# Kernel tuning notes

Measured on AMD Instinct MI355X. Metric: run time of the kernel, lower is better.

Reference implementation:

```python
import jax, jax.numpy as jnp
import numpy as np

D_MODEL = 1024
N_HEADS = 16
HEAD_DIM = D_MODEL // N_HEADS
NEG_INF = -1e9


def setup_inputs() -> dict:
    key = jax.random.key(0)
    ks = jax.random.split(key, 6)
    B, T, C = 4, 2048, D_MODEL
    x = jax.random.normal(ks[0], (B, T, C), dtype=jnp.float32)
    # causal mask, broadcastable over batch and heads
    mask = jnp.tril(jnp.ones((T, T), dtype=jnp.int32))[None, None]
    scale = 1.0 / np.sqrt(C)
    W_qkv = jax.random.normal(ks[1], (3 * C, C), dtype=jnp.float32) * scale
    b_qkv = jnp.zeros((3 * C,), dtype=jnp.float32)
    W_out = jax.random.normal(ks[2], (C, C), dtype=jnp.float32) * scale
    b_out = jnp.zeros((C,), dtype=jnp.float32)
    return {"x": x, "mask": mask, "W_qkv": W_qkv, "b_qkv": b_qkv,
            "W_out": W_out, "b_out": b_out}


def reference(x, mask, W_qkv, b_qkv, W_out, b_out):
    B, T, C = x.shape
    H, D = N_HEADS, HEAD_DIM
    qkv = x @ W_qkv.T + b_qkv                      # [B, T, 3C]
    q, k, v = jnp.split(qkv, 3, axis=-1)
    # [B, T, C] -> [B, H, T, D]
    q = q.reshape(B, T, H, D).transpose(0, 2, 1, 3)
    k = k.reshape(B, T, H, D).transpose(0, 2, 1, 3)
    v = v.reshape(B, T, H, D).transpose(0, 2, 1, 3)
    scores = jnp.einsum("bhqd,bhkd->bhqk", q, k) / np.sqrt(D)
    scores = jnp.where(mask == 0, NEG_INF, scores)
    att = jax.nn.softmax(scores, axis=-1)          # dropout p=0 (eval)
    out = jnp.einsum("bhqk,bhkd->bhqd", att, v)    # [B, H, T, D]
    out = out.transpose(0, 2, 1, 3).reshape(B, T, C)
    return out @ W_out.T + b_out
```

## Files before the change

kernel.cpp:

```cpp
#include <hip/hip_runtime.h>
#include <hip/hip_bf16.h>

typedef unsigned short u16;
typedef unsigned int u32;
using short8 = __attribute__((ext_vector_type(8))) short;
using f32x4  = __attribute__((ext_vector_type(4))) float;
using f32x16 = __attribute__((ext_vector_type(16))) float;
using uint2v = __attribute__((ext_vector_type(2))) u32;

#define T_SEQ 2048
#define C_DIM 1024
#define NH 16
#define HD 64

#if __has_builtin(__builtin_amdgcn_exp2f)
#define EXP2(x) __builtin_amdgcn_exp2f(x)
#else
#define EXP2(x) exp2f(x)
#endif

__device__ __forceinline__ u16 f2bf(float f) {
    unsigned int u = __float_as_uint(f);
    unsigned int r = (u + 0x7fffu + ((u >> 16) & 1u)) >> 16;
    return (u16)r;
}
__device__ __forceinline__ u32 cvtpk(float lo, float hi) {
    u32 r;
    asm("v_cvt_pk_bf16_f32 %0, %1, %2" : "=v"(r) : "v"(lo), "v"(hi));
    return r;
}
__device__ __forceinline__ short8 mk8(u32 a, u32 b, u32 c, u32 d) {
    union { u32 u[4]; short8 s; } t;
    t.u[0] = a; t.u[1] = b; t.u[2] = c; t.u[3] = d;
    return t.s;
}
__device__ __forceinline__ void gl_lds16(const u16* g, u16* l) {
    __builtin_amdgcn_global_load_lds(
        (const __attribute__((address_space(1))) unsigned int*)g,
        (__attribute__((address_space(3))) unsigned int*)l, 16, 0, 0);
}
template <int N> __device__ __forceinline__ void s_vmcnt();
template <> __device__ __forceinline__ void s_vmcnt<0>() {
    asm volatile("s_waitcnt vmcnt(0)" ::: "memory");
}
template <> __device__ __forceinline__ void s_vmcnt<4>() {
    asm volatile("s_waitcnt vmcnt(4)" ::: "memory");
}
__device__ __forceinline__ void BAR() {
    asm volatile("" ::: "memory");
    __builtin_amdgcn_s_barrier();
    asm volatile("" ::: "memory");
}

__global__ __launch_bounds__(256) void cvt_f32_bf16(const float* __restrict__ in,
                                                    u16* __restrict__ out, int n8) {
    int i = blockIdx.x * blockDim.x + threadIdx.x;
    if (i >= n8) return;
    const float4* p = (const float4*)in + (size_t)i * 2;
    float4 a = p[0], b = p[1];
    short8 o;
    o[0] = (short)f2bf(a.x); o[1] = (short)f2bf(a.y);
    o[2] = (short)f2bf(a.z); o[3] = (short)f2bf(a.w);
    o[4] = (short)f2bf(b.x); o[5] = (short)f2bf(b.y);
    o[6] = (short)f2bf(b.z); o[7] = (short)f2bf(b.w);
    *(short8*)(out + (size_t)i * 8) = o;
}

__global__ __launch_bounds__(256) void cvt_w2(const float* __restrict__ a,
                                              u16* __restrict__ oa, int na8,
                                              const float* __restrict__ b,
                                              u16* __restrict__ ob, int nb8) {
    int i = blockIdx.x * blockDim.x + threadIdx.x;
    const float* src;
    u16* dst;
    if (i < na8) { src = a; dst = oa; }
    else if (i < na8 + nb8) { src = b; dst = ob; i -= na8; }
    else return;
    const float4* p = (const float4*)src + (size_t)i * 2;
    float4 x = p[0], y = p[1];
    short8 o;
    o[0] = (short)f2bf(x.x); o[1] = (short)f2bf(x.y);
    o[2] = (short)f2bf(x.z); o[3] = (short)f2bf(x.w);
    o[4] = (short)f2bf(y.x); o[5] = (short)f2bf(y.y);
    o[6] = (short)f2bf(y.z); o[7] = (short)f2bf(y.w);
    *(short8*)(dst + (size_t)i * 8) = o;
}

template <int EPI, int NX>
__global__ __launch_bounds__(256) void gemm_bt(const u16* __restrict__ A,
                                               const u16* __restrict__ Bt,
                                               const float* __restrict__ bias,
                                               u16* __restrict__ qb, u16* __restrict__ kb,
                                               u16* __restrict__ vtb, float* __restrict__ Cf,
                                               int M, int N, int K) {
    __shared__ __align__(16) u16 Al[2][128][32];
    __shared__ __align__(16) u16 Bl[2][128][32];
    const int tid = threadIdx.x;
    const int lane = tid & 63, wid = tid >> 6;
    const int li = lane & 15, g = lane >> 4;
    const int wr = (wid >> 1) * 64, wc = (wid & 1) * 64;

    const int bid = blockIdx.x;
    const int xcd = bid & 7;
    const int r_ = bid >> 3;
    const int xq = r_ >> 5;
    const int rem = r_ & 31;
    const int yloc = rem >> 2, xr = rem & 3;
    const size_t m0 = (size_t)(xcd * 8 + yloc) * 128;
    const size_t n0 = (size_t)(xq * 4 + xr) * 128;

    const int srow = lane >> 2;
    const int sch = (lane & 3) ^ ((srow >> 1) & 3);
    const u16* aA = A + (m0 + wid * 32 + srow) * (size_t)K + sch * 8;
    const u16* aB = Bt + (n0 + wid * 32 + srow) * (size_t)K + sch * 8;

    f32x4 acc[4][4] = {};
    const int nt = K / 32;

    auto STAGE = [&](int buf, int k0) {
        gl_lds16(aA + k0, &Al[buf][wid * 32][0]);
        gl_lds16(aA + 16 * (size_t)K + k0, &Al[buf][wid * 32 + 16][0]);
        gl_lds16(aB + k0, &Bl[buf][wid * 32][0]);
        gl_lds16(aB + 16 * (size_t)K + k0, &Bl[buf][wid * 32 + 16][0]);
    };

    STAGE(0, 0);
#pragma unroll 2
    for (int t = 0; t < nt; ++t) {
        if (t + 1 < nt) { STAGE((t + 1) & 1, (t + 1) * 32); s_vmcnt<4>(); }
        else            { s_vmcnt<0>(); }
        BAR();
        short8 af[4], bf[4];
#pragma unroll
        for (int i = 0; i < 4; i++) {
            int row = wr + i * 16 + li;
            af[i] = *(const short8*)&Al[t & 1][row][(g ^ ((row >> 1) & 3)) * 8];
        }
#pragma unroll
        for (int i = 0; i < 4; i++) {
            int row = wc + i * 16 + li;
            bf[i] = *(const short8*)&Bl[t & 1][row][(g ^ ((row >> 1) & 3)) * 8];
        }
        __builtin_amdgcn_s_setprio(1);
#pragma unroll
        for (int mi = 0; mi < 4; mi++)
#pragma unroll
            for (int ni = 0; ni < 4; ni++)
                acc[mi][ni] = __builtin_amdgcn_mfma_f32_16x16x32_bf16(af[mi], bf[ni],
                                                                      acc[mi][ni], 0, 0, 0);
        __builtin_amdgcn_s_setprio(0);
        BAR();
    }

#pragma unroll
    for (int mi = 0; mi < 4; mi++)
#pragma unroll
        for (int ni = 0; ni < 4; ni++) {
            size_t col = n0 + wc + ni * 16 + li;
            size_t row0 = m0 + wr + mi * 16 + g * 4;
            if (EPI == 0) {
                int which = (int)(col >> 10);
                int rem2 = (int)(col & 1023);
                int h = rem2 >> 6, d = rem2 & 63;
                size_t b = row0 >> 11, t0v = row0 & 2047;
                float bv = bias[col];
                if (which == 2) {
                    ushort4 o4;
                    o4.x = f2bf(acc[mi][ni][0] + bv);
                    o4.y = f2bf(acc[mi][ni][1] + bv);
                    o4.z = f2bf(acc[mi][ni][2] + bv);
                    o4.w = f2bf(acc[mi][ni][3] + bv);
                    *(ushort4*)(vtb + (((b * NH) + h) * (size_t)HD + d) * T_SEQ + t0v) = o4;
                } else {
                    u16* dst = (which == 0) ? qb : kb;
                    float sc = (which == 0) ? 0.18033688f : 1.0f;
#pragma unroll
                    for (int r = 0; r < 4; r++)
                        dst[(((b * NH) + h) * T_SEQ + t0v + r) * HD + d] =
                            f2bf((acc[mi][ni][r] + bv) * sc);
                }
            } else {
                float bv = bias[col];
#pragma unroll
                for (int r = 0; r < 4; r++)
                    Cf[(row0 + r) * (size_t)N + col] = acc[mi][ni][r] + bv;
            }
        }
}

__global__ __launch_bounds__(256) void attn_fwd2(const u16* __restrict__ Q,
                                                 const u16* __restrict__ K,
                                                 const u16* __restrict__ Vt,
                                                 u16* __restrict__ O) {
    __shared__ __align__(16) u16 KL[2][64 * 64];
    __shared__ __align__(16) u16 VL[2][64 * 64];
    const int tid = threadIdx.x;
    const int lane = tid & 63, wid = tid >> 6;
    const int l31 = lane & 31, hi = lane >> 5;

    const int wg = blockIdx.x;
    const int j = wg >> 8, c = wg & 255;
    const int xcd = c & 7, m = c >> 3;
    const int bh = (xcd << 3) | (m >> 2);
    const int v = m & 3;
    const int qt = (j == 0) ? (15 - v) : (j == 1) ? v : (j == 2) ? (11 - v) : (v + 4);

    const size_t bhT = (size_t)bh * T_SEQ;
    const int srow8 = lane >> 3, sch = lane & 7;
    const int b = bh >> 4, h = bh & 15;
    const int x7 = l31 & 7;

    const int q0 = qt * 128;
    const int qw0 = q0 + wid * 32;
    const int nkt = 2 * qt + 2;

    short8 qf[4];
    {
        const u16* qp = Q + (bhT + qw0 + l31) * HD + hi * 8;
#pragma unroll
        for (int s = 0; s < 4; s++) qf[s] = *(const short8*)(qp + s * 16);
    }

    f32x16 o0 = {}, o1 = {};
    float l_run = 0.f;

#pragma unroll
    for (int i = 0; i < 2; i++) {
        int row = wid * 16 + i * 8 + srow8;
        int ch = sch ^ (row & 7);
        gl_lds16(K + (bhT + row) * HD + ch * 8, &KL[0][(wid * 16 + i * 8) * 64]);
        gl_lds16(Vt + ((size_t)bh * HD + row) * T_SEQ + ch * 8,
                 &VL[0][(wid * 16 + i * 8) * 64]);
    }

    for (int kt = 0; kt < nkt; kt++) {
        if (kt + 1 < nkt) {
            const int kv0n = (kt + 1) * 64;
            const int nb = (kt + 1) & 1;
#pragma unroll
            for (int i = 0; i < 2; i++) {
                int row = wid * 16 + i * 8 + srow8;
                int ch = sch ^ (row & 7);
                gl_lds16(K + (bhT + kv0n + row) * HD + ch * 8,
                         &KL[nb][(wid * 16 + i * 8) * 64]);
                gl_lds16(Vt + ((size_t)bh * HD + row) * T_SEQ + kv0n + ch * 8,
                         &VL[nb][(wid * 16 + i * 8) * 64]);
            }
            s_vmcnt<4>();
        } else {
            s_vmcnt<0>();
        }
        BAR();

        const int kv0 = kt * 64;
        if (kv0 <= qw0) {
            const u16* KLb = KL[kt & 1];
            const u16* VLb = VL[kt & 1];

            f32x16 s0 = {}, s1 = {};
            __builtin_amdgcn_s_setprio(1);
#pragma unroll
            for (int sl = 0; sl < 4; sl++) {
                int ch = ((sl * 2 + hi) ^ x7) * 8;
                short8 ka = *(const short8*)&KLb[l31 * 64 + ch];
                s0 = __builtin_amdgcn_mfma_f32_32x32x16_bf16(ka, qf[sl], s0, 0, 0, 0);
                short8 kb2 = *(const short8*)&KLb[(32 + l31) * 64 + ch];
                s1 = __builtin_amdgcn_mfma_f32_32x32x16_bf16(kb2, qf[sl], s1, 0, 0, 0);
            }
            __builtin_amdgcn_s_setprio(0);

            const int qg = qw0 + l31;
            if (kv0 + 63 > qw0) {
#pragma unroll
                for (int r = 0; r < 16; r++) {
                    int kvr = kv0 + (r & 3) + 8 * (r >> 2) + 4 * hi;
                    if (kvr > qg) s0[r] = -1e30f;
                    if (kvr + 32 > qg) s1[r] = -1e30f;
                }
            }

            float ls = 0.f;
#pragma unroll
            for (int r = 0; r < 16; r++) {
                float p0 = EXP2(s0[r]);
                float p1 = EXP2(s1[r]);
                s0[r] = p0; s1[r] = p1;
                ls += p0 + p1;
            }
            ls += __shfl_xor(ls, 32);
            l_run += ls;

            {
                u32 c0 = cvtpk(s0[0], s0[1]),   c1 = cvtpk(s0[2], s0[3]),
                    c2 = cvtpk(s0[4], s0[5]),   c3 = cvtpk(s0[6], s0[7]),
                    c4 = cvtpk(s0[8], s0[9]),   c5 = cvtpk(s0[10], s0[11]),
                    c6 = cvtpk(s0[12], s0[13]), c7 = cvtpk(s0[14], s0[15]);
                uint2v wA = __builtin_amdgcn_permlane32_swap(c0, c2, false, false);
                uint2v wB = __builtin_amdgcn_permlane32_swap(c1, c3, false, false);
                uint2v wC = __builtin_amdgcn_permlane32_swap(c4, c6, false, false);
                uint2v wD = __builtin_amdgcn_permlane32_swap(c5, c7, false, false);
                short8 paA = mk8(wA[0], wB[0], wA[1], wB[1]);
                short8 paB = mk8(wC[0], wD[0], wC[1], wD[1]);
                __builtin_amdgcn_s_setprio(1);
#pragma unroll
                for (int sl = 0; sl < 2; sl++) {
                    short8 pa = (sl == 0) ? paA : paB;
                    int ch = ((sl * 2 + hi) ^ x7) * 8;
                    short8 va = *(const short8*)&VLb[l31 * 64 + ch];
                    o0 = __builtin_amdgcn_mfma_f32_32x32x16_bf16(pa, va, o0, 0, 0, 0);
                    short8 vb2 = *(const short8*)&VLb[(32 + l31) * 64 + ch];
                    o1 = __builtin_amdgcn_mfma_f32_32x32x16_bf16(pa, vb2, o1, 0, 0, 0);
                }
                __builtin_amdgcn_s_setprio(0);
            }
            {
                u32 c0 = cvtpk(s1[0], s1[1]),   c1 = cvtpk(s1[2], s1[3]),
                    c2 = cvtpk(s1[4], s1[5]),   c3 = cvtpk(s1[6], s1[7]),
                    c4 = cvtpk(s1[8], s1[9]),   c5 = cvtpk(s1[10], s1[11]),
                    c6 = cvtpk(s1[12], s1[13]), c7 = cvtpk(s1[14], s1[15]);
                uint2v wA = __builtin_amdgcn_permlane32_swap(c0, c2, false, false);
                uint2v wB = __builtin_amdgcn_permlane32_swap(c1, c3, false, false);
                uint2v wC = __builtin_amdgcn_permlane32_swap(c4, c6, false, false);
                uint2v wD = __builtin_amdgcn_permlane32_swap(c5, c7, false, false);
                short8 paC = mk8(wA[0], wB[0], wA[1], wB[1]);
                short8 paD = mk8(wC[0], wD[0], wC[1], wD[1]);
                __builtin_amdgcn_s_setprio(1);
#pragma unroll
                for (int sl = 2; sl < 4; sl++) {
                    short8 pa = (sl == 2) ? paC : paD;
                    int ch = ((sl * 2 + hi) ^ x7) * 8;
                    short8 va = *(const short8*)&VLb[l31 * 64 + ch];
                    o0 = __builtin_amdgcn_mfma_f32_32x32x16_bf16(pa, va, o0, 0, 0, 0);
                    short8 vb2 = *(const short8*)&VLb[(32 + l31) * 64 + ch];
                    o1 = __builtin_amdgcn_mfma_f32_32x32x16_bf16(pa, vb2, o1, 0, 0, 0);
                }
                __builtin_amdgcn_s_setprio(0);
            }
        }
        BAR();
    }

    const float inv = 1.0f / l_run;
#pragma unroll
    for (int r = 0; r < 16; r++) {
        int qr = (r & 3) + 8 * (r >> 2) + 4 * hi;
        float invr = __shfl(inv, qr);
        int t = q0 + wid * 32 + qr;
        size_t rowoff = ((size_t)b * T_SEQ + t) * C_DIM + h * HD;
        O[rowoff + l31]      = f2bf(o0[r] * invr);
        O[rowoff + 32 + l31] = f2bf(o1[r] * invr);
    }
}

extern "C" void kernel_launch(void* const* d_in, const int* in_sizes, int n_in,
                              void* d_out, int out_size, void* d_ws, size_t ws_size,
                              hipStream_t stream) {
    const float* x     = (const float*)d_in[0];
    const float* W_qkv = (const float*)d_in[2];
    const float* b_qkv = (const float*)d_in[3];
    const float* W_out = (const float*)d_in[4];
    const float* b_out = (const float*)d_in[5];
    float* out = (float*)d_out;

    char* w = (char*)d_ws;
    u16* xb    = (u16*)(w);
    u16* wqkvb = (u16*)(w + 16777216);
    u16* woutb = (u16*)(w + 23068672);
    u16* qb    = (u16*)(w + 25165824);
    u16* kb    = (u16*)(w + 41943040);
    u16* vtb   = (u16*)(w + 58720256);
    u16* attnb = xb;

    cvt_f32_bf16<<<4096, 256, 0, stream>>>(x, xb, 1048576);
    cvt_w2<<<2048, 256, 0, stream>>>(W_qkv, wqkvb, 393216, W_out, woutb, 131072);

    gemm_bt<0, 24><<<1536, 256, 0, stream>>>(xb, wqkvb, b_qkv, qb, kb, vtb, nullptr,
                                             8192, 3072, 1024);

    attn_fwd2<<<1024, 256, 0, stream>>>(qb, kb, vtb, attnb);

    gemm_bt<1, 8><<<512, 256, 0, stream>>>(attnb, woutb, b_out, nullptr, nullptr,
                                           nullptr, out, 8192, 1024, 1024);
}
```

Baseline: 160.0 us.

## Enlarge attention workgroups to 8 waves covering 256 query rows

The attention kernel now launches 512 workgroups of 512 threads, each covering 256 query rows instead of 128, so every K/V tile staged in LDS is reused by twice as many waves. Each wave now issues one K load and one V load per tile rather than two of each, and the wait count is adjusted to match. The causal load-balancing map is simplified to pair tiles v and 7-v. The exponentials for the second score block are moved to after the first PV MFMA block to interleave transcendental and matrix work. The trade-off is more waves sharing each barrier, masked-out waves idling longer in the causal region, and a coarser grid.

```diff
diff --git a/kernel.cpp b/kernel.cpp
--- a/kernel.cpp
+++ b/kernel.cpp
@@ -42,6 +42,9 @@
 template <int N> __device__ __forceinline__ void s_vmcnt();
 template <> __device__ __forceinline__ void s_vmcnt<0>() {
     asm volatile("s_waitcnt vmcnt(0)" ::: "memory");
+}
+template <> __device__ __forceinline__ void s_vmcnt<2>() {
+    asm volatile("s_waitcnt vmcnt(2)" ::: "memory");
 }
 template <> __device__ __forceinline__ void s_vmcnt<4>() {
     asm volatile("s_waitcnt vmcnt(4)" ::: "memory");
@@ -188,7 +191,7 @@
         }
 }
 
-__global__ __launch_bounds__(256) void attn_fwd2(const u16* __restrict__ Q,
+__global__ __launch_bounds__(512) void attn_fwd2(const u16* __restrict__ Q,
                                                  const u16* __restrict__ K,
                                                  const u16* __restrict__ Vt,
                                                  u16* __restrict__ O) {
@@ -203,16 +206,16 @@
     const int xcd = c & 7, m = c >> 3;
     const int bh = (xcd << 3) | (m >> 2);
     const int v = m & 3;
-    const int qt = (j == 0) ? (15 - v) : (j == 1) ? v : (j == 2) ? (11 - v) : (v + 4);
+    const int qt = j ? v : (7 - v);
 
     const size_t bhT = (size_t)bh * T_SEQ;
-    const int srow8 = lane >> 3, sch = lane & 7;
+    const int srow8 = lane >> 3, sch = (lane & 7) ^ srow8;
     const int b = bh >> 4, h = bh & 15;
     const int x7 = l31 & 7;
 
-    const int q0 = qt * 128;
+    const int q0 = qt * 256;
     const int qw0 = q0 + wid * 32;
-    const int nkt = 2 * qt + 2;
+    const int nkt = 4 * qt + 4;
 
     short8 qf[4];
     {
@@ -224,29 +227,19 @@
     f32x16 o0 = {}, o1 = {};
     float l_run = 0.f;
 
-#pragma unroll
-    for (int i = 0; i < 2; i++) {
-        int row = wid * 16 + i * 8 + srow8;
-        int ch = sch ^ (row & 7);
-        gl_lds16(K + (bhT + row) * HD + ch * 8, &KL[0][(wid * 16 + i * 8) * 64]);
-        gl_lds16(Vt + ((size_t)bh * HD + row) * T_SEQ + ch * 8,
-                 &VL[0][(wid * 16 + i * 8) * 64]);
-    }
+    gl_lds16(K + (bhT + wid * 8 + srow8) * HD + sch * 8, &KL[0][wid * 8 * 64]);
+    gl_lds16(Vt + ((size_t)bh * HD + wid * 8 + srow8) * T_SEQ + sch * 8,
+             &VL[0][wid * 8 * 64]);
 
     for (int kt = 0; kt < nkt; kt++) {
         if (kt + 1 < nkt) {
             const int kv0n = (kt + 1) * 64;
             const int nb = (kt + 1) & 1;
-#pragma unroll
-            for (int i = 0; i < 2; i++) {
-                int row = wid * 16 + i * 8 + srow8;
-                int ch = sch ^ (row & 7);
-                gl_lds16(K + (bhT + kv0n + row) * HD + ch * 8,
-                         &KL[nb][(wid * 16 + i * 8) * 64]);
-                gl_lds16(Vt + ((size_t)bh * HD + row) * T_SEQ + kv0n + ch * 8,
-                         &VL[nb][(wid * 16 + i * 8) * 64]);
-            }
-            s_vmcnt<4>();
+            gl_lds16(K + (bhT + kv0n + wid * 8 + srow8) * HD + sch * 8,
+                     &KL[nb][wid * 8 * 64]);
+            gl_lds16(Vt + ((size_t)bh * HD + wid * 8 + srow8) * T_SEQ + kv0n + sch * 8,
+                     &VL[nb][wid * 8 * 64]);
+            s_vmcnt<2>();
         } else {
             s_vmcnt<0>();
         }
@@ -282,14 +275,9 @@
             float ls = 0.f;
 #pragma unroll
             for (int r = 0; r < 16; r++) {
-                float p0 = EXP2(s0[r]);
-                float p1 = EXP2(s1[r]);
-                s0[r] = p0; s1[r] = p1;
-                ls += p0 + p1;
-            }
-            ls += __shfl_xor(ls, 32);
-            l_run += ls;
-
+                float p = EXP2(s0[r]);
+                s0[r] = p; ls += p;
+            }
             {
                 u32 c0 = cvtpk(s0[0], s0[1]),   c1 = cvtpk(s0[2], s0[3]),
                     c2 = cvtpk(s0[4], s0[5]),   c3 = cvtpk(s0[6], s0[7]),
@@ -313,6 +301,11 @@
                 }
                 __builtin_amdgcn_s_setprio(0);
             }
+#pragma unroll
+            for (int r = 0; r < 16; r++) {
+                float p = EXP2(s1[r]);
+                s1[r] = p; ls += p;
+            }
             {
                 u32 c0 = cvtpk(s1[0], s1[1]),   c1 = cvtpk(s1[2], s1[3]),
                     c2 = cvtpk(s1[4], s1[5]),   c3 = cvtpk(s1[6], s1[7]),
@@ -336,6 +329,8 @@
                 }
                 __builtin_amdgcn_s_setprio(0);
             }
+            ls += __shfl_xor(ls, 32);
+            l_run += ls;
         }
         BAR();
     }
@@ -377,7 +372,7 @@
     gemm_bt<0, 24><<<1536, 256, 0, stream>>>(xb, wqkvb, b_qkv, qb, kb, vtb, nullptr,
                                              8192, 3072, 1024);
 
-    attn_fwd2<<<1024, 256, 0, stream>>>(qb, kb, vtb, attnb);
+    attn_fwd2<<<512, 512, 0, stream>>>(qb, kb, vtb, attnb);
 
     gemm_bt<1, 8><<<512, 256, 0, stream>>>(attnb, woutb, b_out, nullptr, nullptr,
                                            nullptr, out, 8192, 1024, 1024);
```

After: 160.3 us. About the same (+0.2%).
